# Optimization experiments

Hardware: AMD Instinct MI355X
Metric: run time of the kernel (lower is better)

Reference implementation:

```python
import jax, jax.numpy as jnp
import numpy as np

TEMPERATURE = 30.0
NUM_KERNELS = 4


def setup_inputs() -> dict:
    key = jax.random.key(0)
    ks = jax.random.split(key, 7)
    B, H, W, C = 32, 56, 56, 256
    F, KH, KW, K = 256, 3, 3, NUM_KERNELS
    hidden = C // 4  # attention_reduction_ratio = 4
    x = jax.random.normal(ks[0], (B, H, W, C), dtype=jnp.float32)
    # K parallel conv kernels (HWIO layout) and biases
    fan = KH * KW * C
    kernels = jax.random.normal(ks[1], (K, KH, KW, C, F), dtype=jnp.float32) / np.sqrt(fan)
    biases = jnp.zeros((K, F), dtype=jnp.float32)
    # attention MLP: GAP -> Dense(C//4, relu) -> Dense(K)
    w1 = jax.random.normal(ks[2], (C, hidden), dtype=jnp.float32) / np.sqrt(C)
    b1 = jnp.zeros((hidden,), dtype=jnp.float32)
    w2 = jax.random.normal(ks[3], (hidden, K), dtype=jnp.float32) / np.sqrt(hidden)
    b2 = jnp.zeros((K,), dtype=jnp.float32)
    return {"x": x, "kernels": kernels, "biases": biases,
            "w1": w1, "b1": b1, "w2": w2, "b2": b2}


def reference(x, kernels, biases, w1, b1, w2, b2):
    # Attention router: GAP -> Dense(relu) -> Dense(K) -> softmax(logits / tau)
    pooled = jnp.mean(x, axis=(1, 2))                       # [B, C]
    h = jax.nn.relu(pooled @ w1 + b1)                       # [B, C//4]
    logits = h @ w2 + b2                                    # [B, K]
    attn = jax.nn.softmax(logits / TEMPERATURE, axis=-1)    # [B, K]

    # K parallel conv branches (stride 1, SAME padding, dilation 1, groups 1)
    def conv_k(w, b):
        y = jax.lax.conv_general_dilated(
            x, w, window_strides=(1, 1), padding='SAME',
            dimension_numbers=('NHWC', 'HWIO', 'NHWC'))
        return y + b                                        # [B, H, W, F]

    ys = jax.vmap(conv_k)(kernels, biases)                  # [K, B, H, W, F]
    # per-sample weighted aggregation of branch outputs
    out = jnp.einsum('kbhwf,bk->bhwf', ys, attn)            # [B, H, W, F]
    return out
```

## Files before the change

kernel.cpp:

```cpp
#include <hip/hip_runtime.h>
#include <hip/hip_bf16.h>
#include <stdint.h>

typedef __bf16 bf16_t;
typedef __bf16 bf16x4 __attribute__((ext_vector_type(4)));
typedef __bf16 bf16x8 __attribute__((ext_vector_type(8)));
typedef float floatx4 __attribute__((ext_vector_type(4)));

#define B_ 32
#define HP 58
#define WP 66

#define XPAD_OFF   0u
#define WAGG_OFF   62717952u
#define POOLED_OFF 100466688u
#define ATTN_OFF   100499456u
#define BIASAGG_OFF 100499968u

__device__ __forceinline__ void async_copy16(const void* gsrc, void* ldst) {
  __builtin_amdgcn_global_load_lds(
      (const __attribute__((address_space(1))) unsigned int*)gsrc,
      (__attribute__((address_space(3))) unsigned int*)ldst, 16, 0, 0);
}

__global__ void pad_pool(const float* __restrict__ x, bf16_t* __restrict__ xpad,
                         float* __restrict__ pooled) {
  const int hp = blockIdx.x;
  const int b  = blockIdx.y;
  const int c  = threadIdx.x;
  const int h  = hp - 1;
  const bool hvalid = (h >= 0) && (h < 56);
  bf16_t* dst = xpad + ((size_t)(b * 58 + hp)) * (66 * 256);
  const float* srcrow = x + ((size_t)(b * 56 + (hvalid ? h : 0))) * (56 * 256);
  float sum = 0.f;
  for (int wp = 0; wp < 66; ++wp) {
    int w = wp - 1;
    float v = 0.f;
    if (hvalid && w >= 0 && w < 56) { v = srcrow[w * 256 + c]; sum += v; }
    dst[wp * 256 + c] = (bf16_t)v;
  }
  if (hvalid) atomicAdd(&pooled[b * 256 + c], sum);
}

__global__ void router(const float* __restrict__ pooled, const float* __restrict__ w1,
                       const float* __restrict__ b1, const float* __restrict__ w2,
                       const float* __restrict__ b2, const float* __restrict__ biases,
                       float* __restrict__ attn, float* __restrict__ biasagg) {
  __shared__ float ps[8192];
  __shared__ float hs[2048];
  __shared__ float lg[128];
  __shared__ float at[128];
  const int t = threadIdx.x;
  for (int i = t; i < 8192; i += 256) ps[i] = pooled[i] * (1.0f / 3136.0f);
  __syncthreads();
  for (int task = t; task < 2048; task += 256) {
    int b = task >> 6, j = task & 63;
    float s = b1[j];
    const float* pb = ps + b * 256;
    for (int c = 0; c < 256; ++c) s += pb[c] * w1[c * 64 + j];
    hs[task] = fmaxf(s, 0.f);
  }
  __syncthreads();
  if (t < 128) {
    int b = t >> 2, k = t & 3;
    float s = b2[k];
    const float* hb = hs + b * 64;
    for (int j = 0; j < 64; ++j) s += hb[j] * w2[j * 4 + k];
    lg[t] = s * (1.0f / 30.0f);
  }
  __syncthreads();
  if (t < 32) {
    int b = t;
    float z0 = lg[b*4], z1 = lg[b*4+1], z2 = lg[b*4+2], z3 = lg[b*4+3];
    float m = fmaxf(fmaxf(z0, z1), fmaxf(z2, z3));
    float e0 = expf(z0-m), e1 = expf(z1-m), e2 = expf(z2-m), e3 = expf(z3-m);
    float inv = 1.0f / (e0 + e1 + e2 + e3);
    at[b*4] = e0*inv; at[b*4+1] = e1*inv; at[b*4+2] = e2*inv; at[b*4+3] = e3*inv;
    attn[b*4] = at[b*4]; attn[b*4+1] = at[b*4+1];
    attn[b*4+2] = at[b*4+2]; attn[b*4+3] = at[b*4+3];
  }
  __syncthreads();
  for (int i = t; i < 8192; i += 256) {
    int b = i >> 8, f = i & 255;
    biasagg[i] = at[b*4]*biases[f] + at[b*4+1]*biases[256+f]
               + at[b*4+2]*biases[512+f] + at[b*4+3]*biases[768+f];
  }
}

__global__ __launch_bounds__(256)
void wagg_kernel(const float* __restrict__ kers, const float* __restrict__ attn,
                 bf16_t* __restrict__ wagg) {
  const int cq  = blockIdx.x;
  const int tap = blockIdx.y;
  const int b   = blockIdx.z;
  const int t   = threadIdx.x;
  __shared__ bf16_t tile[64 * 260];

  const float a0 = attn[b*4+0], a1 = attn[b*4+1], a2 = attn[b*4+2], a3 = attn[b*4+3];
  const float* k0 = kers + ((size_t)(0 * 9 + tap)) * 65536;
  const float* k1 = kers + ((size_t)(1 * 9 + tap)) * 65536;
  const float* k2 = kers + ((size_t)(2 * 9 + tap)) * 65536;
  const float* k3 = kers + ((size_t)(3 * 9 + tap)) * 65536;

  const int fq = t & 63;
  const int cl = t >> 6;
  const int f0 = fq * 4;
#pragma unroll
  for (int pass = 0; pass < 16; ++pass) {
    const int c_local = pass * 4 + cl;
    const size_t o = (size_t)(cq * 64 + c_local) * 256 + f0;
    floatx4 v0 = *(const floatx4*)(k0 + o);
    floatx4 v1 = *(const floatx4*)(k1 + o);
    floatx4 v2 = *(const floatx4*)(k2 + o);
    floatx4 v3 = *(const floatx4*)(k3 + o);
    bf16x4 r;
#pragma unroll
    for (int j = 0; j < 4; ++j)
      r[j] = (bf16_t)(a0 * v0[j] + a1 * v1[j] + a2 * v2[j] + a3 * v3[j]);
    *(bf16x4*)&tile[c_local * 260 + f0] = r;
  }
  __syncthreads();

  bf16_t* wt = wagg + ((size_t)(b * 9 + tap)) * 65536 + cq * 64;
#pragma unroll
  for (int pass = 0; pass < 8; ++pass) {
    const int gi = pass * 256 + t;
    const int f  = gi >> 3;
    const int cg = gi & 7;
    bf16x8 v;
#pragma unroll
    for (int i = 0; i < 8; ++i) v[i] = tile[(cg * 8 + i) * 260 + f];
    *(bf16x8*)(wt + (size_t)f * 256 + cg * 8) = v;
  }
}

#define PBUF_BYTES 20480
#define BBUF_BYTES 16384

__global__ __launch_bounds__(256, 2)
void conv_mfma(const bf16_t* __restrict__ xpad, const bf16_t* __restrict__ wagg,
               const float* __restrict__ biasagg, float* __restrict__ out) {
  __shared__ char lds[2 * PBUF_BYTES + 2 * BBUF_BYTES];
  char* ldsP = lds;
  char* ldsB = lds + 2 * PBUF_BYTES;

  const int tile = blockIdx.x;
  const int b    = blockIdx.y;
  const int h0 = (tile >> 2) * 8;
  const int w0 = (tile & 3) * 14;

  const int tid  = threadIdx.x;
  const int lane = tid & 63;
  const int wv   = tid >> 6;
  const int l15  = lane & 15;
  const int quad = lane >> 4;
  const int n0   = wv * 64;

  const char* xb = (const char*)xpad + (size_t)b * (HP * WP * 256 * 2);
  const char* wb = (const char*)wagg + (size_t)b * (9 * 256 * 256 * 2);

  int offs[7];
#pragma unroll
  for (int mi = 0; mi < 7; ++mi) {
    int m = mi * 16 + l15;
    int ty = m / 14;
    int tx = m - ty * 14;
    offs[mi] = ty * 16 + tx;
  }
  int boff[4];
#pragma unroll
  for (int ni = 0; ni < 4; ++ni) {
    int f = n0 + ni * 16 + l15;
    boff[ni] = f * 64 + ((quad ^ ((f >> 1) & 3)) << 4);
  }

  floatx4 acc[7][4];
#pragma unroll
  for (int mi = 0; mi < 7; ++mi)
#pragma unroll
    for (int ni = 0; ni < 4; ++ni) acc[mi][ni] = (floatx4){0.f, 0.f, 0.f, 0.f};

  auto stage_patch = [&](int cq, int pb) {
#pragma unroll
    for (int ii = 0; ii < 5; ++ii) {
      int i20 = wv * 5 + ii;
      int p = i20 * 8 + (lane >> 3);
      int gsrc = (lane & 7) ^ (p & 7);
      const char* src = xb + ((size_t)((h0 + (p >> 4)) * WP + (w0 + (p & 15))) * 512)
                           + cq * 128 + gsrc * 16;
      async_copy16(src, ldsP + pb * PBUF_BYTES + i20 * 1024);
    }
  };
  auto stage_b = [&](int cq, int tap, int ks, int bb) {
    const char* wt = wb + (size_t)tap * (256 * 256 * 2);
    int kbyte = cq * 128 + ks * 64;
#pragma unroll
    for (int ii = 0; ii < 4; ++ii) {
      int i16 = wv * 4 + ii;
      int f = i16 * 16 + (lane >> 2);
      int gsrc = (lane & 3) ^ ((f >> 1) & 3);
      const char* src = wt + f * 512 + kbyte + gsrc * 16;
      async_copy16(src, ldsB + bb * BBUF_BYTES + i16 * 1024);
    }
  };

  stage_patch(0, 0);
  stage_b(0, 0, 0, 0);
  __syncthreads();

  int step = 0, cq = 0, tap = 0, ks = 0;
  while (true) {
    int nks = ks + 1, ntap = tap, ncq = cq;
    if (nks == 2) { nks = 0; ++ntap; if (ntap == 9) { ntap = 0; ++ncq; } }
    const bool have_next = (ncq < 4);
    if (have_next) {
      stage_b(ncq, ntap, nks, (step + 1) & 1);
      if (ncq != cq) stage_patch(ncq, ncq & 1);
    }
    {
      const char* pc = ldsP + (cq & 1) * PBUF_BYTES;
      const char* bc = ldsB + (step & 1) * BBUF_BYTES;
      const int tapoff = (tap / 3) * 16 + (tap % 3);
      const int gA = ks * 4 + quad;
      bf16x8 a[7];
#pragma unroll
      for (int mi = 0; mi < 7; ++mi) {
        int p = offs[mi] + tapoff;
        int addr = (p << 7) + ((gA ^ (p & 7)) << 4);
        a[mi] = *(const bf16x8*)(pc + addr);
      }
      bf16x8 bv[4];
#pragma unroll
      for (int ni = 0; ni < 4; ++ni) bv[ni] = *(const bf16x8*)(bc + boff[ni]);
#pragma unroll
      for (int mi = 0; mi < 7; ++mi)
#pragma unroll
        for (int ni = 0; ni < 4; ++ni)
          acc[mi][ni] = __builtin_amdgcn_mfma_f32_16x16x32_bf16(a[mi], bv[ni], acc[mi][ni], 0, 0, 0);
    }
    __syncthreads();
    if (!have_next) break;
    cq = ncq; tap = ntap; ks = nks; ++step;
  }

  float bias[4];
#pragma unroll
  for (int ni = 0; ni < 4; ++ni) bias[ni] = biasagg[b * 256 + n0 + ni * 16 + l15];
  float* outb = out + (size_t)b * (56 * 56 * 256);
#pragma unroll
  for (int mi = 0; mi < 7; ++mi) {
#pragma unroll
    for (int rg = 0; rg < 4; ++rg) {
      int m = mi * 16 + quad * 4 + rg;
      int ty = m / 14, tx = m - ty * 14;
      float* orow = outb + ((size_t)((h0 + ty) * 56) + (w0 + tx)) * 256 + n0 + l15;
#pragma unroll
      for (int ni = 0; ni < 4; ++ni) orow[ni * 16] = acc[mi][ni][rg] + bias[ni];
    }
  }
}

extern "C" void kernel_launch(void* const* d_in, const int* in_sizes, int n_in,
                              void* d_out, int out_size, void* d_ws, size_t ws_size,
                              hipStream_t stream) {
  const float* x      = (const float*)d_in[0];
  const float* kers   = (const float*)d_in[1];
  const float* biases = (const float*)d_in[2];
  const float* w1     = (const float*)d_in[3];
  const float* b1     = (const float*)d_in[4];
  const float* w2     = (const float*)d_in[5];
  const float* b2     = (const float*)d_in[6];
  float* outp = (float*)d_out;
  char* ws = (char*)d_ws;

  bf16_t* xpad   = (bf16_t*)(ws + XPAD_OFF);
  bf16_t* wagg   = (bf16_t*)(ws + WAGG_OFF);
  float* pooled  = (float*)(ws + POOLED_OFF);
  float* attn    = (float*)(ws + ATTN_OFF);
  float* biasagg = (float*)(ws + BIASAGG_OFF);

  hipMemsetAsync(pooled, 0, 32 * 256 * sizeof(float), stream);
  pad_pool<<<dim3(58, 32), 256, 0, stream>>>(x, xpad, pooled);
  router<<<1, 256, 0, stream>>>(pooled, w1, b1, w2, b2, biases, attn, biasagg);
  wagg_kernel<<<dim3(4, 9, 32), 256, 0, stream>>>(kers, attn, wagg);
  conv_mfma<<<dim3(28, 32), 256, 0, stream>>>(xpad, wagg, biasagg, outp);
}
```

Before: 389.0 us.

## Load conv weights straight to registers, remap blocks, vectorize pad and split router

The conv kernel stops staging the aggregated weights through LDS. Each lane now loads its B fragments from global memory into registers, double-buffered across k-steps, so a barrier is only needed when the input-patch buffer changes. Block IDs are remapped so that neighbouring blocks work on different batches, which changes L2 locality. pad_pool now uses float4 loads with an LDS reduction before the atomics, and the router MLP's first layer is spread over 8 blocks. The costs are more global-load latency inside the MFMA loop, and an aliasing risk: the hidden-layer buffer shares workspace with biasagg.

```diff
diff --git a/kernel.cpp b/kernel.cpp
--- a/kernel.cpp
+++ b/kernel.cpp
@@ -23,44 +23,62 @@
       (__attribute__((address_space(3))) unsigned int*)ldst, 16, 0, 0);
 }
 
-__global__ void pad_pool(const float* __restrict__ x, bf16_t* __restrict__ xpad,
-                         float* __restrict__ pooled) {
+__global__ __launch_bounds__(256)
+void pad_pool(const float* __restrict__ x, bf16_t* __restrict__ xpad,
+              float* __restrict__ pooled) {
   const int hp = blockIdx.x;
   const int b  = blockIdx.y;
-  const int c  = threadIdx.x;
+  const int t  = threadIdx.x;
+  const int wq = t >> 6, cl = t & 63, c0 = cl * 4;
   const int h  = hp - 1;
   const bool hvalid = (h >= 0) && (h < 56);
   bf16_t* dst = xpad + ((size_t)(b * 58 + hp)) * (66 * 256);
-  const float* srcrow = x + ((size_t)(b * 56 + (hvalid ? h : 0))) * (56 * 256);
-  float sum = 0.f;
-  for (int wp = 0; wp < 66; ++wp) {
+  const float* srow = x + ((size_t)(b * 56 + (hvalid ? h : 0))) * (56 * 256);
+  floatx4 s = {0.f, 0.f, 0.f, 0.f};
+  const int wp0 = wq * 17;
+  const int wpend = (wp0 + 17 < 66) ? wp0 + 17 : 66;
+  for (int wp = wp0; wp < wpend; ++wp) {
     int w = wp - 1;
-    float v = 0.f;
-    if (hvalid && w >= 0 && w < 56) { v = srcrow[w * 256 + c]; sum += v; }
-    dst[wp * 256 + c] = (bf16_t)v;
-  }
-  if (hvalid) atomicAdd(&pooled[b * 256 + c], sum);
-}
-
-__global__ void router(const float* __restrict__ pooled, const float* __restrict__ w1,
-                       const float* __restrict__ b1, const float* __restrict__ w2,
-                       const float* __restrict__ b2, const float* __restrict__ biases,
-                       float* __restrict__ attn, float* __restrict__ biasagg) {
-  __shared__ float ps[8192];
-  __shared__ float hs[2048];
+    floatx4 v = {0.f, 0.f, 0.f, 0.f};
+    if (hvalid && (unsigned)w < 56u) {
+      v = *(const floatx4*)(srow + w * 256 + c0);
+      s += v;
+    }
+    bf16x4 r = {(bf16_t)v.x, (bf16_t)v.y, (bf16_t)v.z, (bf16_t)v.w};
+    *(bf16x4*)(dst + wp * 256 + c0) = r;
+  }
+  __shared__ floatx4 red4[4][64];
+  red4[wq][cl] = s;
+  __syncthreads();
+  if (wq == 0 && hvalid) {
+    floatx4 tot = red4[0][cl] + red4[1][cl] + red4[2][cl] + red4[3][cl];
+    atomicAdd(&pooled[b * 256 + c0 + 0], tot.x);
+    atomicAdd(&pooled[b * 256 + c0 + 1], tot.y);
+    atomicAdd(&pooled[b * 256 + c0 + 2], tot.z);
+    atomicAdd(&pooled[b * 256 + c0 + 3], tot.w);
+  }
+}
+
+__global__ __launch_bounds__(256)
+void router_hidden(const float* __restrict__ pooled, const float* __restrict__ w1,
+                   const float* __restrict__ b1, float* __restrict__ hs) {
+  const int idx = blockIdx.x * 256 + threadIdx.x;
+  const int b = idx >> 6, j = idx & 63;
+  float s = b1[j];
+  const float* pb = pooled + b * 256;
+#pragma unroll 8
+  for (int c = 0; c < 256; ++c)
+    s = fmaf(pb[c] * (1.0f / 3136.0f), w1[c * 64 + j], s);
+  hs[idx] = fmaxf(s, 0.f);
+}
+
+__global__ __launch_bounds__(256)
+void router_tail(const float* __restrict__ hs, const float* __restrict__ w2,
+                 const float* __restrict__ b2, const float* __restrict__ biases,
+                 float* __restrict__ attn, float* __restrict__ biasagg) {
   __shared__ float lg[128];
   __shared__ float at[128];
   const int t = threadIdx.x;
-  for (int i = t; i < 8192; i += 256) ps[i] = pooled[i] * (1.0f / 3136.0f);
-  __syncthreads();
-  for (int task = t; task < 2048; task += 256) {
-    int b = task >> 6, j = task & 63;
-    float s = b1[j];
-    const float* pb = ps + b * 256;
-    for (int c = 0; c < 256; ++c) s += pb[c] * w1[c * 64 + j];
-    hs[task] = fmaxf(s, 0.f);
-  }
-  __syncthreads();
   if (t < 128) {
     int b = t >> 2, k = t & 3;
     float s = b2[k];
@@ -135,17 +153,15 @@
 }
 
 #define PBUF_BYTES 20480
-#define BBUF_BYTES 16384
 
 __global__ __launch_bounds__(256, 2)
 void conv_mfma(const bf16_t* __restrict__ xpad, const bf16_t* __restrict__ wagg,
                const float* __restrict__ biasagg, float* __restrict__ out) {
-  __shared__ char lds[2 * PBUF_BYTES + 2 * BBUF_BYTES];
-  char* ldsP = lds;
-  char* ldsB = lds + 2 * PBUF_BYTES;
-
-  const int tile = blockIdx.x;
-  const int b    = blockIdx.y;
+  __shared__ char ldsP[2 * PBUF_BYTES];
+
+  const int id   = blockIdx.x;
+  const int b    = (id & 7) * 4 + ((id >> 3) / 28);
+  const int tile = (id >> 3) % 28;
   const int h0 = (tile >> 2) * 8;
   const int w0 = (tile & 3) * 14;
 
@@ -158,6 +174,7 @@
 
   const char* xb = (const char*)xpad + (size_t)b * (HP * WP * 256 * 2);
   const char* wb = (const char*)wagg + (size_t)b * (9 * 256 * 256 * 2);
+  const int laneB = (n0 + l15) * 512 + quad * 16;
 
   int offs[7];
 #pragma unroll
@@ -166,12 +183,6 @@
     int ty = m / 14;
     int tx = m - ty * 14;
     offs[mi] = ty * 16 + tx;
-  }
-  int boff[4];
-#pragma unroll
-  for (int ni = 0; ni < 4; ++ni) {
-    int f = n0 + ni * 16 + l15;
-    boff[ni] = f * 64 + ((quad ^ ((f >> 1) & 3)) << 4);
   }
 
   floatx4 acc[7][4];
@@ -191,56 +202,48 @@
       async_copy16(src, ldsP + pb * PBUF_BYTES + i20 * 1024);
     }
   };
-  auto stage_b = [&](int cq, int tap, int ks, int bb) {
-    const char* wt = wb + (size_t)tap * (256 * 256 * 2);
-    int kbyte = cq * 128 + ks * 64;
-#pragma unroll
-    for (int ii = 0; ii < 4; ++ii) {
-      int i16 = wv * 4 + ii;
-      int f = i16 * 16 + (lane >> 2);
-      int gsrc = (lane & 3) ^ ((f >> 1) & 3);
-      const char* src = wt + f * 512 + kbyte + gsrc * 16;
-      async_copy16(src, ldsB + bb * BBUF_BYTES + i16 * 1024);
-    }
+  auto load_b4 = [&](bf16x8* dst, int cq, int tap, int ks) {
+    const char* base = wb + (size_t)tap * 131072 + cq * 128 + ks * 64 + laneB;
+#pragma unroll
+    for (int ni = 0; ni < 4; ++ni)
+      dst[ni] = *(const bf16x8*)(base + ni * 8192);
   };
 
+  bf16x8 bcur[4], bnxt[4];
   stage_patch(0, 0);
-  stage_b(0, 0, 0, 0);
-  __syncthreads();
-
-  int step = 0, cq = 0, tap = 0, ks = 0;
-  while (true) {
-    int nks = ks + 1, ntap = tap, ncq = cq;
-    if (nks == 2) { nks = 0; ++ntap; if (ntap == 9) { ntap = 0; ++ncq; } }
-    const bool have_next = (ncq < 4);
-    if (have_next) {
-      stage_b(ncq, ntap, nks, (step + 1) & 1);
-      if (ncq != cq) stage_patch(ncq, ncq & 1);
-    }
-    {
-      const char* pc = ldsP + (cq & 1) * PBUF_BYTES;
-      const char* bc = ldsB + (step & 1) * BBUF_BYTES;
+  load_b4(bcur, 0, 0, 0);
+  __syncthreads();
+
+  for (int cq = 0; cq < 4; ++cq) {
+    const char* pc = ldsP + (cq & 1) * PBUF_BYTES;
+    for (int tap = 0; tap < 9; ++tap) {
       const int tapoff = (tap / 3) * 16 + (tap % 3);
-      const int gA = ks * 4 + quad;
-      bf16x8 a[7];
-#pragma unroll
-      for (int mi = 0; mi < 7; ++mi) {
-        int p = offs[mi] + tapoff;
-        int addr = (p << 7) + ((gA ^ (p & 7)) << 4);
-        a[mi] = *(const bf16x8*)(pc + addr);
+#pragma unroll
+      for (int ks = 0; ks < 2; ++ks) {
+        const bool last = (tap == 8) && (ks == 1);
+        if (!last) {
+          load_b4(bnxt, cq, tap + ks, ks ^ 1);
+        } else if (cq < 3) {
+          stage_patch(cq + 1, (cq + 1) & 1);
+          load_b4(bnxt, cq + 1, 0, 0);
+        }
+        const int gA = ks * 4 + quad;
+        bf16x8 a[7];
+#pragma unroll
+        for (int mi = 0; mi < 7; ++mi) {
+          int p = offs[mi] + tapoff;
+          a[mi] = *(const bf16x8*)(pc + (p << 7) + ((gA ^ (p & 7)) << 4));
+        }
+#pragma unroll
+        for (int mi = 0; mi < 7; ++mi)
+#pragma unroll
+          for (int ni = 0; ni < 4; ++ni)
+            acc[mi][ni] = __builtin_amdgcn_mfma_f32_16x16x32_bf16(a[mi], bcur[ni], acc[mi][ni], 0, 0, 0);
+#pragma unroll
+        for (int ni = 0; ni < 4; ++ni) bcur[ni] = bnxt[ni];
       }
-      bf16x8 bv[4];
-#pragma unroll
-      for (int ni = 0; ni < 4; ++ni) bv[ni] = *(const bf16x8*)(bc + boff[ni]);
-#pragma unroll
-      for (int mi = 0; mi < 7; ++mi)
-#pragma unroll
-        for (int ni = 0; ni < 4; ++ni)
-          acc[mi][ni] = __builtin_amdgcn_mfma_f32_16x16x32_bf16(a[mi], bv[ni], acc[mi][ni], 0, 0, 0);
-    }
-    __syncthreads();
-    if (!have_next) break;
-    cq = ncq; tap = ntap; ks = nks; ++step;
+    }
+    if (cq < 3) __syncthreads();
   }
 
   float bias[4];
@@ -278,10 +281,12 @@
   float* pooled  = (float*)(ws + POOLED_OFF);
   float* attn    = (float*)(ws + ATTN_OFF);
   float* biasagg = (float*)(ws + BIASAGG_OFF);
+  float* hs      = (float*)(ws + BIASAGG_OFF);
 
   hipMemsetAsync(pooled, 0, 32 * 256 * sizeof(float), stream);
   pad_pool<<<dim3(58, 32), 256, 0, stream>>>(x, xpad, pooled);
-  router<<<1, 256, 0, stream>>>(pooled, w1, b1, w2, b2, biases, attn, biasagg);
+  router_hidden<<<8, 256, 0, stream>>>(pooled, w1, b1, hs);
+  router_tail<<<1, 256, 0, stream>>>(hs, w2, b2, biases, attn, biasagg);
   wagg_kernel<<<dim3(4, 9, 32), 256, 0, stream>>>(kers, attn, wagg);
-  conv_mfma<<<dim3(28, 32), 256, 0, stream>>>(xpad, wagg, biasagg, outp);
-}
+  conv_mfma<<<896, 256, 0, stream>>>(xpad, wagg, biasagg, outp);
+}
```

Result: slower. 614.1 us (+57.9%).
